# Performance work log

Hardware: AMD Instinct MI355X
Metric: run time of the kernel (lower is better)

## Reference

```python
import jax, jax.numpy as jnp
import numpy as np

DIM = 1024
HEADS = 16
HEAD_DIM = DIM // HEADS
SCALE = HEAD_DIM ** -0.5


def setup_inputs() -> dict:
    key = jax.random.key(0)
    ks = jax.random.split(key, 5)
    B, N, C = 2, 2048, DIM
    x = jax.random.normal(ks[0], (B, N, C), dtype=jnp.float32)
    x2 = jax.random.normal(ks[1], (B, N, C), dtype=jnp.float32)
    # torch nn.Linear weights: [out_features, in_features], no bias (qkv_bias=False)
    s = (1.0 / C) ** 0.5
    Wq = jax.random.uniform(ks[2], (C, C), jnp.float32, -s, s)
    Wa = jax.random.uniform(ks[3], (C, C), jnp.float32, -s, s)
    Wkv = jax.random.uniform(ks[4], (2 * C, C), jnp.float32, -s, s)
    return {"x": x, "x2": x2, "Wq": Wq, "Wa": Wa, "Wkv": Wkv}


def reference(x, x2, Wq, Wa, Wkv):
    B, N, C = x.shape
    H, D = HEADS, HEAD_DIM

    def heads(t):  # [B,N,C] -> [B,H,N,D]
        return t.reshape(B, N, H, D).transpose(0, 2, 1, 3)

    q = heads(x @ Wq.T)
    A = heads(x2 @ Wa.T)
    kv = (x @ Wkv.T).reshape(B, N, 2, H, D).transpose(2, 0, 3, 1, 4)
    k, v = kv[0], kv[1]

    # cascaded double attention (dropout layers in eval mode = identity)
    ATT_q = jax.nn.softmax(jnp.einsum('bhnd,bhmd->bhnm', q, A) * SCALE, axis=-1)
    ATT_k = jax.nn.softmax(jnp.einsum('bhnd,bhmd->bhnm', A, k) * SCALE, axis=-1)
    out = jnp.einsum('bhnm,bhmd->bhnd', ATT_q,
                     jnp.einsum('bhnm,bhmd->bhnd', ATT_k, v))
    return out.transpose(0, 2, 1, 3).reshape(B, N, C)
```

## Files before the change

kernel.cpp:

```cpp
#include <hip/hip_runtime.h>

#define DIM 1024
#define HEADS 16
#define HDIM 64
#define SEQ 2048
#define SCLOG2 0.18033688011112042f

typedef __attribute__((ext_vector_type(8))) short short8;
typedef __attribute__((ext_vector_type(4))) float f32x4;
typedef __attribute__((ext_vector_type(16))) float f32x16;
typedef __attribute__((ext_vector_type(4))) int i32x4;

static __device__ __forceinline__ unsigned short f2bf(float f){
  union { float f; unsigned int u; } v; v.f = f;
  unsigned int r = v.u + 0x7fffu + ((v.u >> 16) & 1u);
  return (unsigned short)(r >> 16);
}

static __device__ __forceinline__ int cvtpk(float lo, float hi){
  int r;
  asm("v_cvt_pk_bf16_f32 %0, %1, %2" : "=v"(r) : "v"(lo), "v"(hi));
  return r;
}
static __device__ __forceinline__ void swap32(int& a, int& b){
  asm("v_permlane32_swap_b32 %0, %1" : "+v"(a), "+v"(b));
}

__device__ __forceinline__ void gl_lds16(const unsigned short* g, unsigned short* l){
  __builtin_amdgcn_global_load_lds((const __attribute__((address_space(1))) void*)g,
                                   (__attribute__((address_space(3))) void*)l, 16, 0, 0);
}

#define CAST_TOTAL 3145728

__global__ __launch_bounds__(256)
void cast_all(const float* __restrict__ x, const float* __restrict__ x2,
              const float* __restrict__ wq, const float* __restrict__ wa,
              const float* __restrict__ wkv, unsigned short* __restrict__ out)
{
  for (int i = blockIdx.x*256 + threadIdx.x; i < CAST_TOTAL; i += gridDim.x*256){
    const float* src; int off;
    if      (i < 1048576){ src = x;   off = i; }
    else if (i < 2097152){ src = x2;  off = i - 1048576; }
    else if (i < 2359296){ src = wq;  off = i - 2097152; }
    else if (i < 2621440){ src = wa;  off = i - 2359296; }
    else                 { src = wkv; off = i - 2621440; }
    float4 v = ((const float4*)src)[off];
    ushort4 o;
    o.x = f2bf(v.x); o.y = f2bf(v.y); o.z = f2bf(v.z); o.w = f2bf(v.w);
    ((ushort4*)out)[i] = o;
  }
}

#define GK 1024

__global__ __launch_bounds__(256)
void gemm_all(const unsigned short* __restrict__ xb,  const unsigned short* __restrict__ x2b,
              const unsigned short* __restrict__ Wqb, const unsigned short* __restrict__ Wab,
              const unsigned short* __restrict__ Wkvb,
              unsigned short* __restrict__ Qw, unsigned short* __restrict__ Aw,
              unsigned short* __restrict__ Kw, unsigned short* __restrict__ Vwt)
{
  __shared__ unsigned short Ald[2][128*64];
  __shared__ unsigned short Bld[2][128*64];
  const int tid  = threadIdx.x;
  const int lane = tid & 63;
  const int wid  = tid >> 6;
  const int l15 = lane & 15, l4 = lane >> 4;
  const int wm = wid >> 1, wn = wid & 1;

  const int bid = blockIdx.x;
  const unsigned short *Abuf, *Bbuf;
  int mbase, nbase, isA;
  if (bid < 768){
    int xcd = bid & 7, s = bid >> 3;
    int mb = xcd*4 + (s & 3);
    int nb = s >> 2;
    nbase = nb*128; mbase = mb*128; isA = 0;
    Abuf = xb;
    Bbuf = (nbase < 1024) ? (Wqb + (size_t)nbase*GK) : (Wkvb + (size_t)(nbase-1024)*GK);
  } else {
    int b2 = bid - 768;
    int xcd = b2 & 7, s = b2 >> 3;
    int mb = xcd*4 + (s & 3);
    int nb = s >> 2;
    nbase = nb*128; mbase = mb*128; isA = 1;
    Abuf = x2b;
    Bbuf = Wab + (size_t)nbase*GK;
  }
  const bool isV = (!isA) && (nbase >= 2048);

  const int srow = wid*32 + (lane >> 3);
  const int scol = ((lane & 7) ^ (lane >> 3)) * 8;
  const unsigned short* gA = Abuf + (size_t)(mbase + srow)*GK + scol;
  const unsigned short* gB = Bbuf + (size_t)srow*GK + scol;

  const int rsw = (l15 & 7) * 8;

  f32x4 acc[4][4];
  #pragma unroll
  for (int i=0;i<4;i++)
    #pragma unroll
    for(int j=0;j<4;j++) acc[i][j] = (f32x4){0.f,0.f,0.f,0.f};

  #pragma unroll
  for (int i=0;i<4;++i){
    gl_lds16(gA + (size_t)(i*8)*GK, &Ald[0][(wid*32 + i*8)*64]);
    gl_lds16(gB + (size_t)(i*8)*GK, &Bld[0][(wid*32 + i*8)*64]);
  }
  asm volatile("s_waitcnt vmcnt(0)" ::: "memory");
  __builtin_amdgcn_s_barrier();
  __builtin_amdgcn_sched_barrier(0);

  for (int t = 0; t < 16; ++t){
    const int cur = t & 1;
    if (t+1 < 16){
      const int nxt = cur ^ 1;
      const int kt = (t+1)*64;
      #pragma unroll
      for (int i=0;i<4;++i){
        gl_lds16(gA + (size_t)(i*8)*GK + kt, &Ald[nxt][(wid*32 + i*8)*64]);
        gl_lds16(gB + (size_t)(i*8)*GK + kt, &Bld[nxt][(wid*32 + i*8)*64]);
      }
    }
    #pragma unroll
    for (int kc = 0; kc < 2; ++kc){
      short8 af[4], bf[4];
      #pragma unroll
      for (int mt=0; mt<4; ++mt)
        af[mt] = *(const short8*)(&Ald[cur][(wm*64 + mt*16 + l15)*64 + ((kc*32 + l4*8) ^ rsw)]);
      #pragma unroll
      for (int nt=0; nt<4; ++nt)
        bf[nt] = *(const short8*)(&Bld[cur][(wn*64 + nt*16 + l15)*64 + ((kc*32 + l4*8) ^ rsw)]);
      __builtin_amdgcn_s_setprio(1);
      if (isV){
        #pragma unroll
        for (int mt=0; mt<4; ++mt)
          #pragma unroll
          for (int nt=0; nt<4; ++nt)
            acc[mt][nt] = __builtin_amdgcn_mfma_f32_16x16x32_bf16(af[mt], bf[nt], acc[mt][nt], 0,0,0);
      } else {
        #pragma unroll
        for (int mt=0; mt<4; ++mt)
          #pragma unroll
          for (int nt=0; nt<4; ++nt)
            acc[mt][nt] = __builtin_amdgcn_mfma_f32_16x16x32_bf16(bf[nt], af[mt], acc[mt][nt], 0,0,0);
      }
      __builtin_amdgcn_s_setprio(0);
    }
    asm volatile("s_waitcnt vmcnt(0)" ::: "memory");
    __builtin_amdgcn_s_barrier();
    __builtin_amdgcn_sched_barrier(0);
  }

  if (!isV){
    unsigned short* dst = isA ? Aw : (nbase < 1024 ? Qw : Kw);
    const int coff = (!isA && nbase >= 1024) ? 1024 : 0;
    const float scale = isA ? SCLOG2 : 1.0f;
    #pragma unroll
    for (int mt=0; mt<4; ++mt){
      int token = mbase + wm*64 + mt*16 + l15;
      int b = token >> 11, n = token & 2047;
      #pragma unroll
      for (int nt=0; nt<4; ++nt){
        int colb = nbase - coff + wn*64 + nt*16 + l4*4;
        int h = colb >> 6, d = colb & 63;
        ushort4 pk;
        pk.x = f2bf(acc[mt][nt][0] * scale);
        pk.y = f2bf(acc[mt][nt][1] * scale);
        pk.z = f2bf(acc[mt][nt][2] * scale);
        pk.w = f2bf(acc[mt][nt][3] * scale);
        *(ushort4*)(dst + ((size_t)((b*HEADS + h)*SEQ + n))*HDIM + d) = pk;
      }
    }
  } else {
    #pragma unroll
    for (int mt=0; mt<4; ++mt){
      int mrow = mbase + wm*64 + mt*16 + l4*4;
      int b = mrow >> 11, nblk = mrow & 2047;
      #pragma unroll
      for (int nt=0; nt<4; ++nt){
        int col = nbase + wn*64 + nt*16 + l15;
        int c2 = col - 2048, h = c2 >> 6, d = c2 & 63;
        ushort4 pk;
        pk.x = f2bf(acc[mt][nt][0]);
        pk.y = f2bf(acc[mt][nt][1]);
        pk.z = f2bf(acc[mt][nt][2]);
        pk.w = f2bf(acc[mt][nt][3]);
        *(ushort4*)(Vwt + ((size_t)((b*HEADS + h)*HDIM + d))*SEQ + nblk) = pk;
      }
    }
  }
}

#define KT2 32
#define NTH 32

__global__ __launch_bounds__(512)
void attn_pass(const unsigned short* __restrict__ Qb,
               const unsigned short* __restrict__ Kb,
               const unsigned short* __restrict__ Vtb,
               unsigned short* __restrict__ ytb,
               float* __restrict__ outf,
               int mode)
{
  __shared__ __align__(16) char SHRAW[65536];
  unsigned short* SH = (unsigned short*)SHRAW;
  const int tid = threadIdx.x, lane = tid & 63, wid = tid >> 6;
  const int l31 = lane & 31, l5 = lane >> 5;
  const int qw = wid & 3, kvh = wid >> 2;

  const int bid = blockIdx.x;
  const int cx = bid & 7, j = bid >> 3;
  const int bh = cx*4 + (j >> 4);
  const int qb = j & 15;
  const int q0 = qb*128 + qw*32;
  const size_t base = (size_t)bh * SEQ * HDIM;

  short8 qf[4];
  #pragma unroll
  for (int db=0; db<4; ++db)
    qf[db] = *(const short8*)(Qb + base + (size_t)(q0 + l31)*HDIM + db*16 + l5*8);

  const unsigned short* gsrc[2];
  int ldst[2];
  int sstep;
  const int grpoff = kvh * 16384;
  if (qw < 2){
    #pragma unroll
    for (int f=0; f<2; ++f){
      gsrc[f] = Kb + base + (size_t)(kvh*1024 + l31)*HDIM + (qw*2 + f)*16 + l5*8;
      ldst[f] = grpoff + (qw*2 + f)*512;
    }
    sstep = KT2*HDIM;
  } else {
    const int db2 = qw - 2;
    #pragma unroll
    for (int f=0; f<2; ++f){
      gsrc[f] = Vtb + base + (size_t)(db2*32 + l31)*SEQ + kvh*1024 + f*16 + l5*8;
      ldst[f] = grpoff + 2048 + (db2*2 + f)*512;
    }
    sstep = KT2;
  }

  f32x16 oo0, oo1;
  #pragma unroll
  for (int r=0;r<16;++r){ oo0[r]=0.f; oo1[r]=0.f; }
  float os[4] = {0.f, 0.f, 0.f, 0.f};

  #pragma unroll
  for (int b=0; b<2; ++b)
    #pragma unroll
    for (int f=0; f<2; ++f)
      gl_lds16(gsrc[f] + (size_t)b*sstep, SH + ldst[f] + b*4096);
  asm volatile("s_waitcnt vmcnt(0)" ::: "memory");
  __builtin_amdgcn_s_barrier();
  __builtin_amdgcn_sched_barrier(0);

  for (int i = 0; i < 16; ++i){
    const int pairBase = (i & 1) * 8192;
    if (i < 15){
      const int stBase = pairBase ^ 8192;
      #pragma unroll
      for (int u=0; u<2; ++u)
        #pragma unroll
        for (int f=0; f<2; ++f)
          gl_lds16(gsrc[f] + (size_t)(2*i+2+u)*sstep, SH + ldst[f] + stBase + u*4096);
    }

    #pragma unroll
    for (int u=0; u<2; ++u){
      const unsigned short* Kc = SH + grpoff + pairBase + u*4096;
      const unsigned short* Vc = Kc + 2048;

      f32x16 sacc;
      #pragma unroll
      for (int r=0;r<16;++r) sacc[r]=0.f;
      __builtin_amdgcn_s_setprio(1);
      #pragma unroll
      for (int db=0; db<4; ++db){
        short8 kfr = *(const short8*)(Kc + db*512 + lane*8);
        sacc = __builtin_amdgcn_mfma_f32_32x32x16_bf16(kfr, qf[db], sacc, 0,0,0);
      }
      __builtin_amdgcn_s_setprio(0);
      float p[16];
      #pragma unroll
      for (int r=0;r<16;++r){
        p[r] = __builtin_amdgcn_exp2f(sacc[r]);
        os[r & 3] += p[r];
      }

      #pragma unroll
      for (int kb2=0; kb2<2; ++kb2){
        const int pb2 = kb2*8;
        int a0 = cvtpk(p[pb2+0], p[pb2+1]);
        int b0 = cvtpk(p[pb2+4], p[pb2+5]);
        int a1 = cvtpk(p[pb2+2], p[pb2+3]);
        int b1 = cvtpk(p[pb2+6], p[pb2+7]);
        swap32(a0, b0);
        swap32(a1, b1);
        i32x4 pav; pav[0]=a0; pav[1]=a1; pav[2]=b0; pav[3]=b1;
        short8 paf = *(short8*)&pav;
        __builtin_amdgcn_s_setprio(1);
        short8 v0 = *(const short8*)(Vc + (0*2+kb2)*512 + lane*8);
        oo0 = __builtin_amdgcn_mfma_f32_32x32x16_bf16(v0, paf, oo0, 0,0,0);
        short8 v1 = *(const short8*)(Vc + (1*2+kb2)*512 + lane*8);
        oo1 = __builtin_amdgcn_mfma_f32_32x32x16_bf16(v1, paf, oo1, 0,0,0);
        __builtin_amdgcn_s_setprio(0);
      }
    }

    if (i < 15){
      asm volatile("s_waitcnt vmcnt(0)" ::: "memory");
    }
    __builtin_amdgcn_s_barrier();
    __builtin_amdgcn_sched_barrier(0);
  }

  float osum = (os[0]+os[1]) + (os[2]+os[3]);
  osum += __shfl_xor(osum, 32);

  float* Of  = (float*)SHRAW;
  float* Os1 = (float*)(SHRAW + 128*68*4);
  const int ql = qw*32 + l31;

  if (kvh == 1){
    #pragma unroll
    for (int g=0; g<4; ++g){
      f32x4 w0, w1;
      #pragma unroll
      for (int r=0;r<4;++r){ w0[r] = oo0[g*4+r]; w1[r] = oo1[g*4+r]; }
      int d0 = 8*g + 4*l5;
      *(f32x4*)(Of + ql*68 + d0)      = w0;
      *(f32x4*)(Of + ql*68 + d0 + 32) = w1;
    }
    Os1[ql] = osum;
  }
  __syncthreads();

  if (kvh == 0){
    const float rinv = 1.0f / (osum + Os1[ql]);
    if (mode == 0){
      #pragma unroll
      for (int r=0;r<16;++r){
        int d0 = (r&3) + 8*(r>>2) + 4*l5;
        float f0 = (oo0[r] + Of[ql*68 + d0])      * rinv;
        float f1 = (oo1[r] + Of[ql*68 + d0 + 32]) * rinv;
        ytb[base + (size_t)(d0)*SEQ + q0 + l31]    = f2bf(f0);
        ytb[base + (size_t)(d0+32)*SEQ + q0 + l31] = f2bf(f1);
      }
    } else {
      #pragma unroll
      for (int g=0; g<4; ++g){
        int d0 = 8*g + 4*l5;
        f32x4 w0 = *(const f32x4*)(Of + ql*68 + d0);
        f32x4 w1 = *(const f32x4*)(Of + ql*68 + d0 + 32);
        #pragma unroll
        for (int r=0;r<4;++r){ w0[r] = (w0[r]+oo0[g*4+r])*rinv; w1[r] = (w1[r]+oo1[g*4+r])*rinv; }
        *(f32x4*)(Of + ql*68 + d0)      = w0;
        *(f32x4*)(Of + ql*68 + d0 + 32) = w1;
      }
    }
  }

  if (mode == 1){
    __syncthreads();
    const int b = bh >> 4, h = bh & 15;
    const int qr = tid >> 2, dh = (tid & 3)*16;
    const float* src = Of + qr*68 + dh;
    float* drow = outf + ((size_t)(b*SEQ + qb*128 + qr))*DIM + h*HDIM + dh;
    #pragma unroll
    for (int k2=0;k2<4;++k2)
      *(float4*)(drow + k2*4) = *(const float4*)(src + k2*4);
  }
}

extern "C" void kernel_launch(void* const* d_in, const int* in_sizes, int n_in,
                              void* d_out, int out_size, void* d_ws, size_t ws_size,
                              hipStream_t stream) {
  const float* x   = (const float*)d_in[0];
  const float* x2  = (const float*)d_in[1];
  const float* Wq  = (const float*)d_in[2];
  const float* Wa  = (const float*)d_in[3];
  const float* Wkv = (const float*)d_in[4];
  float* out = (float*)d_out;

  unsigned short* ws = (unsigned short*)d_ws;
  unsigned short* xb   = ws;
  unsigned short* x2b  = xb   + 4096*1024;
  unsigned short* Wqb  = x2b  + 4096*1024;
  unsigned short* Wab  = Wqb  + 1024*1024;
  unsigned short* Wkvb = Wab  + 1024*1024;
  unsigned short* Qw   = Wkvb + 2048*1024;
  unsigned short* Aw   = Qw   + 4194304;
  unsigned short* Kw   = Aw   + 4194304;
  unsigned short* Vwt  = Kw   + 4194304;
  unsigned short* Ywt  = xb;

  cast_all<<<dim3(3072), dim3(256), 0, stream>>>(x, x2, Wq, Wa, Wkv, ws);

  gemm_all<<<dim3(1024), dim3(256), 0, stream>>>(xb, x2b, Wqb, Wab, Wkvb, Qw, Aw, Kw, Vwt);

  attn_pass<<<dim3(512), dim3(512), 0, stream>>>(Aw, Kw, Vwt, Ywt, nullptr, 0);

  attn_pass<<<dim3(512), dim3(512), 0, stream>>>(Qw, Aw, Ywt, nullptr, out, 1);
}
```

Measured before the change: 146.8 us.

## Fuse fp32-to-bf16 input cast into projection GEMM via register-staged loads

Removes the separate cast kernel and has the projection GEMM load fp32 activations and weights directly into registers, convert them to bf16 with packed converts, and store them swizzled into LDS. This drops the bf16 staging round trip through global memory and one kernel launch. In exchange the GEMM reads twice the bytes per tile, repeats the weight and activation conversion across every tile that reuses them, and replaces the async global-to-LDS path with register-staged loads that raise register pressure.

New measurement: 149.2 us. About the same (+1.7%).

```diff
diff --git a/kernel.cpp b/kernel.cpp
--- a/kernel.cpp
+++ b/kernel.cpp
@@ -31,33 +31,12 @@
                                    (__attribute__((address_space(3))) void*)l, 16, 0, 0);
 }
 
-#define CAST_TOTAL 3145728
+#define GK 1024
 
 __global__ __launch_bounds__(256)
-void cast_all(const float* __restrict__ x, const float* __restrict__ x2,
-              const float* __restrict__ wq, const float* __restrict__ wa,
-              const float* __restrict__ wkv, unsigned short* __restrict__ out)
-{
-  for (int i = blockIdx.x*256 + threadIdx.x; i < CAST_TOTAL; i += gridDim.x*256){
-    const float* src; int off;
-    if      (i < 1048576){ src = x;   off = i; }
-    else if (i < 2097152){ src = x2;  off = i - 1048576; }
-    else if (i < 2359296){ src = wq;  off = i - 2097152; }
-    else if (i < 2621440){ src = wa;  off = i - 2359296; }
-    else                 { src = wkv; off = i - 2621440; }
-    float4 v = ((const float4*)src)[off];
-    ushort4 o;
-    o.x = f2bf(v.x); o.y = f2bf(v.y); o.z = f2bf(v.z); o.w = f2bf(v.w);
-    ((ushort4*)out)[i] = o;
-  }
-}
-
-#define GK 1024
-
-__global__ __launch_bounds__(256)
-void gemm_all(const unsigned short* __restrict__ xb,  const unsigned short* __restrict__ x2b,
-              const unsigned short* __restrict__ Wqb, const unsigned short* __restrict__ Wab,
-              const unsigned short* __restrict__ Wkvb,
+void gemm_all(const float* __restrict__ xf,  const float* __restrict__ x2f,
+              const float* __restrict__ Wqf, const float* __restrict__ Waf,
+              const float* __restrict__ Wkvf,
               unsigned short* __restrict__ Qw, unsigned short* __restrict__ Aw,
               unsigned short* __restrict__ Kw, unsigned short* __restrict__ Vwt)
 {
@@ -70,30 +49,31 @@
   const int wm = wid >> 1, wn = wid & 1;
 
   const int bid = blockIdx.x;
-  const unsigned short *Abuf, *Bbuf;
+  const float *Abuf, *Bbuf;
   int mbase, nbase, isA;
   if (bid < 768){
     int xcd = bid & 7, s = bid >> 3;
     int mb = xcd*4 + (s & 3);
     int nb = s >> 2;
     nbase = nb*128; mbase = mb*128; isA = 0;
-    Abuf = xb;
-    Bbuf = (nbase < 1024) ? (Wqb + (size_t)nbase*GK) : (Wkvb + (size_t)(nbase-1024)*GK);
+    Abuf = xf;
+    Bbuf = (nbase < 1024) ? (Wqf + (size_t)nbase*GK) : (Wkvf + (size_t)(nbase-1024)*GK);
   } else {
     int b2 = bid - 768;
     int xcd = b2 & 7, s = b2 >> 3;
     int mb = xcd*4 + (s & 3);
     int nb = s >> 2;
     nbase = nb*128; mbase = mb*128; isA = 1;
-    Abuf = x2b;
-    Bbuf = Wab + (size_t)nbase*GK;
+    Abuf = x2f;
+    Bbuf = Waf + (size_t)nbase*GK;
   }
   const bool isV = (!isA) && (nbase >= 2048);
 
-  const int srow = wid*32 + (lane >> 3);
-  const int scol = ((lane & 7) ^ (lane >> 3)) * 8;
-  const unsigned short* gA = Abuf + (size_t)(mbase + srow)*GK + scol;
-  const unsigned short* gB = Bbuf + (size_t)srow*GK + scol;
+  const int lrow = lane >> 3;
+  const int c8   = lane & 7;
+  const float* gA = Abuf + (size_t)(mbase + wid*32 + lrow)*GK + c8*8;
+  const float* gB = Bbuf + (size_t)(wid*32 + lrow)*GK + c8*8;
+  const int wslot = (c8 ^ lrow) * 8;
 
   const int rsw = (l15 & 7) * 8;
 
@@ -103,24 +83,38 @@
     #pragma unroll
     for(int j=0;j<4;j++) acc[i][j] = (f32x4){0.f,0.f,0.f,0.f};
 
+  float4 ra[4][2], rb[4][2];
+
   #pragma unroll
   for (int i=0;i<4;++i){
-    gl_lds16(gA + (size_t)(i*8)*GK, &Ald[0][(wid*32 + i*8)*64]);
-    gl_lds16(gB + (size_t)(i*8)*GK, &Bld[0][(wid*32 + i*8)*64]);
-  }
-  asm volatile("s_waitcnt vmcnt(0)" ::: "memory");
-  __builtin_amdgcn_s_barrier();
-  __builtin_amdgcn_sched_barrier(0);
+    ra[i][0] = *(const float4*)(gA + (size_t)(i*8)*GK);
+    ra[i][1] = *(const float4*)(gA + (size_t)(i*8)*GK + 4);
+    rb[i][0] = *(const float4*)(gB + (size_t)(i*8)*GK);
+    rb[i][1] = *(const float4*)(gB + (size_t)(i*8)*GK + 4);
+  }
+  #pragma unroll
+  for (int i=0;i<4;++i){
+    const int roff = (wid*32 + lrow + i*8)*64 + wslot;
+    i32x4 va, vb;
+    va[0] = cvtpk(ra[i][0].x, ra[i][0].y); va[1] = cvtpk(ra[i][0].z, ra[i][0].w);
+    va[2] = cvtpk(ra[i][1].x, ra[i][1].y); va[3] = cvtpk(ra[i][1].z, ra[i][1].w);
+    *(i32x4*)(&Ald[0][roff]) = va;
+    vb[0] = cvtpk(rb[i][0].x, rb[i][0].y); vb[1] = cvtpk(rb[i][0].z, rb[i][0].w);
+    vb[2] = cvtpk(rb[i][1].x, rb[i][1].y); vb[3] = cvtpk(rb[i][1].z, rb[i][1].w);
+    *(i32x4*)(&Bld[0][roff]) = vb;
+  }
+  __syncthreads();
 
   for (int t = 0; t < 16; ++t){
     const int cur = t & 1;
-    if (t+1 < 16){
-      const int nxt = cur ^ 1;
+    if (t < 15){
       const int kt = (t+1)*64;
       #pragma unroll
       for (int i=0;i<4;++i){
-        gl_lds16(gA + (size_t)(i*8)*GK + kt, &Ald[nxt][(wid*32 + i*8)*64]);
-        gl_lds16(gB + (size_t)(i*8)*GK + kt, &Bld[nxt][(wid*32 + i*8)*64]);
+        ra[i][0] = *(const float4*)(gA + (size_t)(i*8)*GK + kt);
+        ra[i][1] = *(const float4*)(gA + (size_t)(i*8)*GK + kt + 4);
+        rb[i][0] = *(const float4*)(gB + (size_t)(i*8)*GK + kt);
+        rb[i][1] = *(const float4*)(gB + (size_t)(i*8)*GK + kt + 4);
       }
     }
     #pragma unroll
@@ -148,9 +142,21 @@
       }
       __builtin_amdgcn_s_setprio(0);
     }
-    asm volatile("s_waitcnt vmcnt(0)" ::: "memory");
-    __builtin_amdgcn_s_barrier();
-    __builtin_amdgcn_sched_barrier(0);
+    if (t < 15){
+      const int nxt = cur ^ 1;
+      #pragma unroll
+      for (int i=0;i<4;++i){
+        const int roff = (wid*32 + lrow + i*8)*64 + wslot;
+        i32x4 va, vb;
+        va[0] = cvtpk(ra[i][0].x, ra[i][0].y); va[1] = cvtpk(ra[i][0].z, ra[i][0].w);
+        va[2] = cvtpk(ra[i][1].x, ra[i][1].y); va[3] = cvtpk(ra[i][1].z, ra[i][1].w);
+        *(i32x4*)(&Ald[nxt][roff]) = va;
+        vb[0] = cvtpk(rb[i][0].x, rb[i][0].y); vb[1] = cvtpk(rb[i][0].z, rb[i][0].w);
+        vb[2] = cvtpk(rb[i][1].x, rb[i][1].y); vb[3] = cvtpk(rb[i][1].z, rb[i][1].w);
+        *(i32x4*)(&Bld[nxt][roff]) = vb;
+      }
+    }
+    __syncthreads();
   }
 
   if (!isV){
@@ -387,19 +393,13 @@
 
   unsigned short* ws = (unsigned short*)d_ws;
   unsigned short* xb   = ws;
-  unsigned short* x2b  = xb   + 4096*1024;
-  unsigned short* Wqb  = x2b  + 4096*1024;
-  unsigned short* Wab  = Wqb  + 1024*1024;
-  unsigned short* Wkvb = Wab  + 1024*1024;
-  unsigned short* Qw   = Wkvb + 2048*1024;
+  unsigned short* Qw   = ws + 8*1024*1024 + 4*1024*1024;
   unsigned short* Aw   = Qw   + 4194304;
   unsigned short* Kw   = Aw   + 4194304;
   unsigned short* Vwt  = Kw   + 4194304;
   unsigned short* Ywt  = xb;
 
-  cast_all<<<dim3(3072), dim3(256), 0, stream>>>(x, x2, Wq, Wa, Wkv, ws);
-
-  gemm_all<<<dim3(1024), dim3(256), 0, stream>>>(xb, x2b, Wqb, Wab, Wkvb, Qw, Aw, Kw, Vwt);
+  gemm_all<<<dim3(1024), dim3(256), 0, stream>>>(x, x2, Wq, Wa, Wkv, Qw, Aw, Kw, Vwt);
 
   attn_pass<<<dim3(512), dim3(512), 0, stream>>>(Aw, Kw, Vwt, Ywt, nullptr, 0);
 
```

## Load K/V fragments directly from global memory, dropping LDS staging in attention

Applied to the files above, without the earlier changes.

The attention pass no longer stages K and V^T tiles through LDS with async global-to-LDS loads, double buffering and barriers. Each wave now reads its MFMA operands straight from global memory, relying on cache hits. Blocks shrink to 256 threads covering 64 query rows, with twice as many blocks and far less shared memory, which raises occupancy and removes barrier stalls. The cost is redundant global and L2 traffic, since K/V are no longer shared across waves through LDS, and load latency is exposed because there is no prefetch pipeline.

Result: slower. 296.7 us (+102.1%).

```diff
diff --git a/kernel.cpp b/kernel.cpp
--- a/kernel.cpp
+++ b/kernel.cpp
@@ -193,10 +193,9 @@
   }
 }
 
-#define KT2 32
-#define NTH 32
-
-__global__ __launch_bounds__(512)
+#define NTQ 32
+
+__global__ __launch_bounds__(256)
 void attn_pass(const unsigned short* __restrict__ Qb,
                const unsigned short* __restrict__ Kb,
                const unsigned short* __restrict__ Vtb,
@@ -204,17 +203,16 @@
                float* __restrict__ outf,
                int mode)
 {
-  __shared__ __align__(16) char SHRAW[65536];
-  unsigned short* SH = (unsigned short*)SHRAW;
+  __shared__ __align__(16) char SHRAW[17664];
   const int tid = threadIdx.x, lane = tid & 63, wid = tid >> 6;
   const int l31 = lane & 31, l5 = lane >> 5;
-  const int qw = wid & 3, kvh = wid >> 2;
+  const int qw = wid & 1, kvh = wid >> 1;
 
   const int bid = blockIdx.x;
   const int cx = bid & 7, j = bid >> 3;
-  const int bh = cx*4 + (j >> 4);
-  const int qb = j & 15;
-  const int q0 = qb*128 + qw*32;
+  const int bh = cx*4 + (j >> 5);
+  const int qb = j & 31;
+  const int q0 = qb*64 + qw*32;
   const size_t base = (size_t)bh * SEQ * HDIM;
 
   short8 qf[4];
@@ -222,106 +220,60 @@
   for (int db=0; db<4; ++db)
     qf[db] = *(const short8*)(Qb + base + (size_t)(q0 + l31)*HDIM + db*16 + l5*8);
 
-  const unsigned short* gsrc[2];
-  int ldst[2];
-  int sstep;
-  const int grpoff = kvh * 16384;
-  if (qw < 2){
-    #pragma unroll
-    for (int f=0; f<2; ++f){
-      gsrc[f] = Kb + base + (size_t)(kvh*1024 + l31)*HDIM + (qw*2 + f)*16 + l5*8;
-      ldst[f] = grpoff + (qw*2 + f)*512;
-    }
-    sstep = KT2*HDIM;
-  } else {
-    const int db2 = qw - 2;
-    #pragma unroll
-    for (int f=0; f<2; ++f){
-      gsrc[f] = Vtb + base + (size_t)(db2*32 + l31)*SEQ + kvh*1024 + f*16 + l5*8;
-      ldst[f] = grpoff + 2048 + (db2*2 + f)*512;
-    }
-    sstep = KT2;
-  }
+  const unsigned short* kq = Kb  + base + (size_t)(kvh*1024 + l31)*HDIM + l5*8;
+  const unsigned short* vq = Vtb + base + (size_t)l31*SEQ + kvh*1024 + l5*8;
 
   f32x16 oo0, oo1;
   #pragma unroll
   for (int r=0;r<16;++r){ oo0[r]=0.f; oo1[r]=0.f; }
   float os[4] = {0.f, 0.f, 0.f, 0.f};
 
-  #pragma unroll
-  for (int b=0; b<2; ++b)
-    #pragma unroll
-    for (int f=0; f<2; ++f)
-      gl_lds16(gsrc[f] + (size_t)b*sstep, SH + ldst[f] + b*4096);
-  asm volatile("s_waitcnt vmcnt(0)" ::: "memory");
-  __builtin_amdgcn_s_barrier();
-  __builtin_amdgcn_sched_barrier(0);
-
-  for (int i = 0; i < 16; ++i){
-    const int pairBase = (i & 1) * 8192;
-    if (i < 15){
-      const int stBase = pairBase ^ 8192;
-      #pragma unroll
-      for (int u=0; u<2; ++u)
-        #pragma unroll
-        for (int f=0; f<2; ++f)
-          gl_lds16(gsrc[f] + (size_t)(2*i+2+u)*sstep, SH + ldst[f] + stBase + u*4096);
-    }
-
-    #pragma unroll
-    for (int u=0; u<2; ++u){
-      const unsigned short* Kc = SH + grpoff + pairBase + u*4096;
-      const unsigned short* Vc = Kc + 2048;
-
-      f32x16 sacc;
-      #pragma unroll
-      for (int r=0;r<16;++r) sacc[r]=0.f;
-      __builtin_amdgcn_s_setprio(1);
-      #pragma unroll
-      for (int db=0; db<4; ++db){
-        short8 kfr = *(const short8*)(Kc + db*512 + lane*8);
-        sacc = __builtin_amdgcn_mfma_f32_32x32x16_bf16(kfr, qf[db], sacc, 0,0,0);
-      }
-      __builtin_amdgcn_s_setprio(0);
-      float p[16];
-      #pragma unroll
-      for (int r=0;r<16;++r){
-        p[r] = __builtin_amdgcn_exp2f(sacc[r]);
-        os[r & 3] += p[r];
-      }
-
-      #pragma unroll
-      for (int kb2=0; kb2<2; ++kb2){
-        const int pb2 = kb2*8;
-        int a0 = cvtpk(p[pb2+0], p[pb2+1]);
-        int b0 = cvtpk(p[pb2+4], p[pb2+5]);
-        int a1 = cvtpk(p[pb2+2], p[pb2+3]);
-        int b1 = cvtpk(p[pb2+6], p[pb2+7]);
-        swap32(a0, b0);
-        swap32(a1, b1);
-        i32x4 pav; pav[0]=a0; pav[1]=a1; pav[2]=b0; pav[3]=b1;
-        short8 paf = *(short8*)&pav;
-        __builtin_amdgcn_s_setprio(1);
-        short8 v0 = *(const short8*)(Vc + (0*2+kb2)*512 + lane*8);
-        oo0 = __builtin_amdgcn_mfma_f32_32x32x16_bf16(v0, paf, oo0, 0,0,0);
-        short8 v1 = *(const short8*)(Vc + (1*2+kb2)*512 + lane*8);
-        oo1 = __builtin_amdgcn_mfma_f32_32x32x16_bf16(v1, paf, oo1, 0,0,0);
-        __builtin_amdgcn_s_setprio(0);
-      }
-    }
-
-    if (i < 15){
-      asm volatile("s_waitcnt vmcnt(0)" ::: "memory");
-    }
-    __builtin_amdgcn_s_barrier();
-    __builtin_amdgcn_sched_barrier(0);
+  for (int t = 0; t < NTQ; ++t){
+    const unsigned short* kt = kq + (size_t)t*32*HDIM;
+    short8 kf0 = *(const short8*)(kt);
+    short8 kf1 = *(const short8*)(kt + 16);
+    short8 kf2 = *(const short8*)(kt + 32);
+    short8 kf3 = *(const short8*)(kt + 48);
+
+    f32x16 sacc;
+    #pragma unroll
+    for (int r=0;r<16;++r) sacc[r]=0.f;
+    sacc = __builtin_amdgcn_mfma_f32_32x32x16_bf16(kf0, qf[0], sacc, 0,0,0);
+    sacc = __builtin_amdgcn_mfma_f32_32x32x16_bf16(kf1, qf[1], sacc, 0,0,0);
+    sacc = __builtin_amdgcn_mfma_f32_32x32x16_bf16(kf2, qf[2], sacc, 0,0,0);
+    sacc = __builtin_amdgcn_mfma_f32_32x32x16_bf16(kf3, qf[3], sacc, 0,0,0);
+
+    float p[16];
+    #pragma unroll
+    for (int r=0;r<16;++r){
+      p[r] = __builtin_amdgcn_exp2f(sacc[r]);
+      os[r & 3] += p[r];
+    }
+
+    const unsigned short* vt = vq + t*32;
+    #pragma unroll
+    for (int kb2=0; kb2<2; ++kb2){
+      const int pb2 = kb2*8;
+      int a0 = cvtpk(p[pb2+0], p[pb2+1]);
+      int b0 = cvtpk(p[pb2+4], p[pb2+5]);
+      int a1 = cvtpk(p[pb2+2], p[pb2+3]);
+      int b1 = cvtpk(p[pb2+6], p[pb2+7]);
+      swap32(a0, b0);
+      swap32(a1, b1);
+      i32x4 pav; pav[0]=a0; pav[1]=a1; pav[2]=b0; pav[3]=b1;
+      short8 paf = *(short8*)&pav;
+      short8 v0 = *(const short8*)(vt + kb2*16);
+      oo0 = __builtin_amdgcn_mfma_f32_32x32x16_bf16(v0, paf, oo0, 0,0,0);
+      short8 v1 = *(const short8*)(vt + (size_t)32*SEQ + kb2*16);
+      oo1 = __builtin_amdgcn_mfma_f32_32x32x16_bf16(v1, paf, oo1, 0,0,0);
+    }
   }
 
   float osum = (os[0]+os[1]) + (os[2]+os[3]);
   osum += __shfl_xor(osum, 32);
 
   float* Of  = (float*)SHRAW;
-  float* Os1 = (float*)(SHRAW + 128*68*4);
+  float* Os1 = (float*)(SHRAW + 64*68*4);
   const int ql = qw*32 + l31;
 
   if (kvh == 1){
@@ -351,14 +303,10 @@
       }
     } else {
       #pragma unroll
-      for (int g=0; g<4; ++g){
-        int d0 = 8*g + 4*l5;
-        f32x4 w0 = *(const f32x4*)(Of + ql*68 + d0);
-        f32x4 w1 = *(const f32x4*)(Of + ql*68 + d0 + 32);
-        #pragma unroll
-        for (int r=0;r<4;++r){ w0[r] = (w0[r]+oo0[g*4+r])*rinv; w1[r] = (w1[r]+oo1[g*4+r])*rinv; }
-        *(f32x4*)(Of + ql*68 + d0)      = w0;
-        *(f32x4*)(Of + ql*68 + d0 + 32) = w1;
+      for (int r=0;r<16;++r){
+        int d0 = (r&3) + 8*(r>>2) + 4*l5;
+        Of[ql*68 + d0]      = (oo0[r] + Of[ql*68 + d0])      * rinv;
+        Of[ql*68 + d0 + 32] = (oo1[r] + Of[ql*68 + d0 + 32]) * rinv;
       }
     }
   }
@@ -368,7 +316,7 @@
     const int b = bh >> 4, h = bh & 15;
     const int qr = tid >> 2, dh = (tid & 3)*16;
     const float* src = Of + qr*68 + dh;
-    float* drow = outf + ((size_t)(b*SEQ + qb*128 + qr))*DIM + h*HDIM + dh;
+    float* drow = outf + ((size_t)(b*SEQ + qb*64 + qr))*DIM + h*HDIM + dh;
     #pragma unroll
     for (int k2=0;k2<4;++k2)
       *(float4*)(drow + k2*4) = *(const float4*)(src + k2*4);
@@ -401,7 +349,7 @@
 
   gemm_all<<<dim3(1024), dim3(256), 0, stream>>>(xb, x2b, Wqb, Wab, Wkvb, Qw, Aw, Kw, Vwt);
 
-  attn_pass<<<dim3(512), dim3(512), 0, stream>>>(Aw, Kw, Vwt, Ywt, nullptr, 0);
-
-  attn_pass<<<dim3(512), dim3(512), 0, stream>>>(Qw, Aw, Ywt, nullptr, out, 1);
-}
+  attn_pass<<<dim3(1024), dim3(256), 0, stream>>>(Aw, Kw, Vwt, Ywt, nullptr, 0);
+
+  attn_pass<<<dim3(1024), dim3(256), 0, stream>>>(Qw, Aw, Ywt, nullptr, out, 1);
+}
```
